# Performance work log

Hardware: AMD Instinct MI355X
Metric: run time of the kernel (lower is better)

## Reference

```python
import jax, jax.numpy as jnp
import numpy as np


def setup_inputs() -> dict:
    key = jax.random.key(0)
    k1, k2, k3, k4 = jax.random.split(key, 4)
    B, Lq, Lk, d = 8, 2048, 2048, 64
    queries = jax.random.normal(k1, (B, Lq, d), dtype=jnp.float32)
    keys = jax.random.normal(k2, (B, Lk, d), dtype=jnp.float32)
    values = jax.random.normal(k3, (B, Lk, d), dtype=jnp.float32)
    valid_lens = jax.random.randint(k4, (B,), 0, 2048, dtype=jnp.int64)
    return {"queries": queries, "keys": keys, "values": values, "valid_lens": valid_lens}


def reference(queries, keys, values, valid_lens):
    # scores: [B, Lq, Lk]
    d = queries.shape[-1]
    scale = 1.0 / jnp.sqrt(jnp.asarray(d, dtype=queries.dtype))
    scores = jnp.einsum("bqd,bkd->bqk", queries, keys) * scale
    # length mask: key positions >= valid_len[b] get -1e6 (as in sequence_mask)
    Lk = keys.shape[1]
    mask = jnp.arange(Lk)[None, None, :] < valid_lens[:, None, None]  # [B,1,Lk]
    scores = jnp.where(mask, scores, jnp.asarray(-1e6, dtype=scores.dtype))
    attn = jax.nn.softmax(scores, axis=-1)
    # dropout p=0.0 -> identity
    return jnp.einsum("bqk,bkd->bqd", attn, values)
```

## Files before the change

### kernel.cpp

```cpp
#include <hip/hip_runtime.h>
#include <hip/hip_bf16.h>
#include <math.h>

typedef __attribute__((ext_vector_type(8))) short short8;
typedef __attribute__((ext_vector_type(16))) float f32x16;

#define DHEAD 64
#define KVB 32
#define QB 32
#define NW 8
#define NWF 4

__device__ __forceinline__ unsigned pack2_bf16(float a, float b) {
  unsigned ua = __builtin_bit_cast(unsigned, a);
  unsigned ub = __builtin_bit_cast(unsigned, b);
  ua = (ua + 0x7fffu + ((ua >> 16) & 1u)) >> 16;
  ub = (ub + 0x7fffu + ((ub >> 16) & 1u)) >> 16;
  return (ua & 0xffffu) | (ub << 16);
}

union Frag { unsigned u[4]; short8 s; };

__global__ __launch_bounds__(256)
void prep_kv(const float* __restrict__ K, const float* __restrict__ V,
             unsigned short* __restrict__ Kf, unsigned short* __restrict__ Vf,
             const int* __restrict__ VL, int Lk) {
  __shared__ float Vs[32][65];
  const int b = blockIdx.y, t = blockIdx.x, tid = threadIdx.x;
  const int LkT = Lk / 32;
  const int vl = VL[b];
  int nkb = (vl == 0) ? LkT : ((vl + 31) / 32);
  if (nkb > LkT) nkb = LkT;
  if (t >= nkb) return;

  const int kk = tid >> 6, lane = tid & 63;
  const int row = lane & 31, colb = kk * 16 + ((lane >> 5) & 1) * 8;
  const size_t base = ((size_t)b * Lk + t * 32) * DHEAD;

  {
    const float* src = K + base + (size_t)row * DHEAD + colb;
    Frag fr;
    #pragma unroll
    for (int j = 0; j < 4; ++j)
      fr.u[j] = pack2_bf16(src[2 * j], src[2 * j + 1]);
    *(short8*)(Kf + ((size_t)(b * LkT + t)) * 2048 + tid * 8) = fr.s;
  }
  for (int e = tid; e < 32 * DHEAD; e += 256) Vs[e >> 6][e & 63] = V[base + e];
  __syncthreads();
  const int region = tid >> 6;
  const int vkk = region & 1, half = region >> 1;
  const int krow = vkk * 16 + ((lane >> 5) & 1) * 8;
  const int d = half * 32 + (lane & 31);
  Frag fv;
  #pragma unroll
  for (int j = 0; j < 4; ++j)
    fv.u[j] = pack2_bf16(Vs[krow + 2 * j][d], Vs[krow + 2 * j + 1][d]);
  *(short8*)(Vf + ((size_t)(b * LkT + t)) * 2048 + tid * 8) = fv.s;
}

__device__ __forceinline__ void tile_body(
    int t, int nkb, int vl, int lane, int hi,
    const unsigned short* __restrict__ kb, const unsigned short* __restrict__ vb,
    const short8 (&qf)[4], short8 (&kc)[4], short8 (&kn)[4],
    short8 (&vc)[4], short8 (&vn)[4],
    f32x16& o0, f32x16& o1, float& m, float& l) {
  const float MASKV = -1442695.04f;

  f32x16 s = {};
  __builtin_amdgcn_s_setprio(1);
  #pragma unroll
  for (int kk = 0; kk < 4; ++kk)
    s = __builtin_amdgcn_mfma_f32_32x32x16_bf16(kc[kk], qf[kk], s, 0, 0, 0);
  __builtin_amdgcn_s_setprio(0);

  const int tn = t + NW;
  if (tn < nkb) {
    const unsigned short* ktn = kb + (size_t)tn * 2048;
    const unsigned short* vtn = vb + (size_t)tn * 2048;
    #pragma unroll
    for (int kk = 0; kk < 4; ++kk) {
      kn[kk] = *(const short8*)(ktn + kk * 512 + lane * 8);
      vn[kk] = *(const short8*)(vtn + kk * 512 + lane * 8);
    }
  }

  const int key0 = t * KVB;
  if (key0 + KVB > vl) {
    #pragma unroll
    for (int r = 0; r < 16; ++r) {
      const int key = key0 + (r & 3) + 8 * (r >> 2) + 4 * hi;
      if (key >= vl) s[r] = MASKV;
    }
  }

  float t0 = fmaxf(s[0], s[1]),  t1 = fmaxf(s[2], s[3]);
  float t2 = fmaxf(s[4], s[5]),  t3 = fmaxf(s[6], s[7]);
  float t4 = fmaxf(s[8], s[9]),  t5 = fmaxf(s[10], s[11]);
  float t6 = fmaxf(s[12], s[13]), t7 = fmaxf(s[14], s[15]);
  t0 = fmaxf(t0, t1); t2 = fmaxf(t2, t3); t4 = fmaxf(t4, t5); t6 = fmaxf(t6, t7);
  t0 = fmaxf(t0, t2); t4 = fmaxf(t4, t6);
  float tm = fmaxf(t0, t4);
  tm = fmaxf(tm, __shfl_xor(tm, 32));

  if (__any(tm > m)) {
    const float mnew  = fmaxf(m, tm);
    const float alpha = exp2f(m - mnew);
    #pragma unroll
    for (int r = 0; r < 16; ++r) { o0[r] *= alpha; o1[r] *= alpha; }
    l *= alpha;
    m = mnew;
  }
  #pragma unroll
  for (int r = 0; r < 16; ++r) s[r] = exp2f(s[r] - m);
  float u0 = s[0] + s[1],  u1 = s[2] + s[3];
  float u2 = s[4] + s[5],  u3 = s[6] + s[7];
  float u4 = s[8] + s[9],  u5 = s[10] + s[11];
  float u6 = s[12] + s[13], u7 = s[14] + s[15];
  u0 += u1; u2 += u3; u4 += u5; u6 += u7; u0 += u2; u4 += u6;
  l += u0 + u4 + __shfl_xor(u0 + u4, 32);

  short8 pf[2];
  #pragma unroll
  for (int kk = 0; kk < 2; ++kk) {
    const unsigned A0 = pack2_bf16(s[8 * kk + 0], s[8 * kk + 1]);
    const unsigned B0 = pack2_bf16(s[8 * kk + 2], s[8 * kk + 3]);
    const unsigned C0 = pack2_bf16(s[8 * kk + 4], s[8 * kk + 5]);
    const unsigned D0 = pack2_bf16(s[8 * kk + 6], s[8 * kk + 7]);
    const unsigned sA = (unsigned)__shfl_xor((int)A0, 32);
    const unsigned sB = (unsigned)__shfl_xor((int)B0, 32);
    const unsigned sC = (unsigned)__shfl_xor((int)C0, 32);
    const unsigned sD = (unsigned)__shfl_xor((int)D0, 32);
    Frag fr;
    fr.u[0] = hi ? sC : A0;
    fr.u[1] = hi ? sD : B0;
    fr.u[2] = hi ? C0 : sA;
    fr.u[3] = hi ? D0 : sB;
    pf[kk] = fr.s;
  }

  __builtin_amdgcn_s_setprio(1);
  o0 = __builtin_amdgcn_mfma_f32_32x32x16_bf16(vc[0], pf[0], o0, 0, 0, 0);
  o1 = __builtin_amdgcn_mfma_f32_32x32x16_bf16(vc[2], pf[0], o1, 0, 0, 0);
  o0 = __builtin_amdgcn_mfma_f32_32x32x16_bf16(vc[1], pf[1], o0, 0, 0, 0);
  o1 = __builtin_amdgcn_mfma_f32_32x32x16_bf16(vc[3], pf[1], o1, 0, 0, 0);
  __builtin_amdgcn_s_setprio(0);
}

__global__ __launch_bounds__(NW * 64, 2)
void fa8(const float* __restrict__ Qg, const unsigned short* __restrict__ Kf,
         const unsigned short* __restrict__ Vf, const int* __restrict__ VL,
         float* __restrict__ Og, int Lq, int Lk, int nqt) {
  __shared__ float OLs[4][QB][DHEAD + 1];
  __shared__ float mL[4][QB];
  __shared__ float lL[4][QB];
  __shared__ float FIN[QB][DHEAD + 2];

  const int tid  = threadIdx.x;
  const int w    = tid >> 6;
  const int lane = tid & 63;
  const int l31  = lane & 31;
  const int hi   = lane >> 5;
  const int qt   = blockIdx.x;
  const int b    = blockIdx.y;
  const int vl   = VL[b];

  const int LkT = Lk / KVB;
  int nkb = (vl == 0) ? LkT : ((vl + KVB - 1) / KVB);
  if (nkb > LkT) nkb = LkT;

  const float cQ = 0.125f * 1.4426950408889634f;
  short8 qf[4];
  {
    const float* qrow = Qg + ((size_t)b * Lq + qt * QB + l31) * DHEAD + hi * 8;
    #pragma unroll
    for (int kk = 0; kk < 4; ++kk) {
      Frag fr;
      #pragma unroll
      for (int j = 0; j < 4; ++j)
        fr.u[j] = pack2_bf16(qrow[kk * 16 + 2 * j] * cQ,
                             qrow[kk * 16 + 2 * j + 1] * cQ);
      qf[kk] = fr.s;
    }
  }

  const unsigned short* kb = Kf + (size_t)b * LkT * 2048;
  const unsigned short* vb = Vf + (size_t)b * LkT * 2048;

  f32x16 o0 = {};
  f32x16 o1 = {};
  float m = -INFINITY;
  float l = 0.0f;

  int t = w;
  if (t < nkb) {
    short8 kA[4], kB[4], vA[4], vB[4];
    const unsigned short* kt = kb + (size_t)t * 2048;
    const unsigned short* vt = vb + (size_t)t * 2048;
    #pragma unroll
    for (int kk = 0; kk < 4; ++kk) {
      kA[kk] = *(const short8*)(kt + kk * 512 + lane * 8);
      vA[kk] = *(const short8*)(vt + kk * 512 + lane * 8);
    }
    while (true) {
      tile_body(t, nkb, vl, lane, hi, kb, vb, qf, kA, kB, vA, vB, o0, o1, m, l);
      t += NW; if (t >= nkb) break;
      tile_body(t, nkb, vl, lane, hi, kb, vb, qf, kB, kA, vB, vA, o0, o1, m, l);
      t += NW; if (t >= nkb) break;
    }
  }

  #pragma unroll
  for (int ph = 0; ph < 3; ++ph) {
    const int wlo  = (ph == 0) ? 4 : (ph == 1) ? 2 : 1;
    const int wcnt = wlo == 1 ? 1 : wlo;

    if (w >= wlo && w < wlo + wcnt) {
      const int s = w - wlo;
      if (hi == 0) { mL[s][l31] = m; lL[s][l31] = l; }
      #pragma unroll
      for (int r = 0; r < 16; ++r) {
        const int dr = (r & 3) + 8 * (r >> 2) + 4 * hi;
        OLs[s][l31][dr]      = o0[r];
        OLs[s][l31][dr + 32] = o1[r];
      }
    }
    __syncthreads();
    if (w < wcnt) {
      const int s = w;
      const float m2 = mL[s][l31];
      const float l2 = lL[s][l31];
      const float M  = fmaxf(m, m2);
      const float a  = (l  > 0.f) ? exp2f(m - M)  : 0.f;
      const float a2 = (l2 > 0.f) ? exp2f(m2 - M) : 0.f;
      #pragma unroll
      for (int r = 0; r < 16; ++r) {
        const int dr = (r & 3) + 8 * (r >> 2) + 4 * hi;
        o0[r] = o0[r] * a + OLs[s][l31][dr]      * a2;
        o1[r] = o1[r] * a + OLs[s][l31][dr + 32] * a2;
      }
      l = l * a + l2 * a2;
      m = M;
    }
    __syncthreads();
  }

  if (w == 0) {
    const float rl = (l > 0.f) ? 1.0f / l : 0.0f;
    #pragma unroll
    for (int r = 0; r < 16; ++r) {
      const int dr = (r & 3) + 8 * (r >> 2) + 4 * hi;
      FIN[l31][dr]      = o0[r] * rl;
      FIN[l31][dr + 32] = o1[r] * rl;
    }
  }
  __syncthreads();
  const size_t base = ((size_t)b * Lq + (size_t)qt * QB) * DHEAD;
  for (int e = tid; e < QB * DHEAD; e += NW * 64)
    Og[base + e] = FIN[e >> 6][e & 63];
}

__global__ __launch_bounds__(NWF * 64)
void fa_fwd(const float* __restrict__ Qg, const float* __restrict__ Kg,
            const float* __restrict__ Vg, const int* __restrict__ VL,
            float* __restrict__ Og, int Lq, int Lk) {
  __shared__ float OLs[NWF][QB][DHEAD + 1];
  __shared__ float mLs[NWF][QB];
  __shared__ float lLs[NWF][QB];

  const int tid  = threadIdx.x;
  const int w    = tid >> 6;
  const int lane = tid & 63;
  const int l31  = lane & 31;
  const int hi   = lane >> 5;
  const int q0   = blockIdx.x * QB;
  const int b    = blockIdx.y;
  const int vl   = VL[b];

  const float* Qb = Qg + (size_t)b * Lq * DHEAD;
  const float* Kb = Kg + (size_t)b * Lk * DHEAD;
  const float* Vb = Vg + (size_t)b * Lk * DHEAD;

  const float cQ = 0.125f * 1.4426950408889634f;
  short8 qf[4];
  {
    const float* qrow = Qb + (size_t)(q0 + l31) * DHEAD + hi * 8;
    #pragma unroll
    for (int kk = 0; kk < 4; ++kk) {
      Frag fr;
      #pragma unroll
      for (int j = 0; j < 4; ++j)
        fr.u[j] = pack2_bf16(qrow[kk * 16 + 2 * j] * cQ,
                             qrow[kk * 16 + 2 * j + 1] * cQ);
      qf[kk] = fr.s;
    }
  }

  f32x16 o0 = {};
  f32x16 o1 = {};
  float m = -INFINITY;
  float l = 0.0f;

  int nkb = (vl == 0) ? (Lk / KVB) : ((vl + KVB - 1) / KVB);
  if (nkb > Lk / KVB) nkb = Lk / KVB;
  const int nt = (nkb > w) ? ((nkb - w + NWF - 1) / NWF) : 0;

  const float MASKV = -1442695.04f;

  float kraw[32], vraw[32];

  if (nt > 0) {
    const float* krow = Kb + (size_t)(w * KVB + l31) * DHEAD + hi * 8;
    #pragma unroll
    for (int kk = 0; kk < 4; ++kk)
      #pragma unroll
      for (int j = 0; j < 8; ++j) kraw[kk * 8 + j] = krow[kk * 16 + j];
  }

  for (int t = 0; t < nt; ++t) {
    const int key0 = (w + t * NWF) * KVB;

    short8 kf[4];
    #pragma unroll
    for (int kk = 0; kk < 4; ++kk) {
      Frag fr;
      #pragma unroll
      for (int j = 0; j < 4; ++j)
        fr.u[j] = pack2_bf16(kraw[kk * 8 + 2 * j], kraw[kk * 8 + 2 * j + 1]);
      kf[kk] = fr.s;
    }

    #pragma unroll
    for (int kk = 0; kk < 2; ++kk) {
      const float* vrow = Vb + (size_t)(key0 + kk * 16 + hi * 8) * DHEAD + l31;
      #pragma unroll
      for (int j = 0; j < 8; ++j) {
        vraw[kk * 16 + j]     = vrow[j * DHEAD];
        vraw[kk * 16 + 8 + j] = vrow[j * DHEAD + 32];
      }
    }

    f32x16 s = {};
    #pragma unroll
    for (int kk = 0; kk < 4; ++kk)
      s = __builtin_amdgcn_mfma_f32_32x32x16_bf16(kf[kk], qf[kk], s, 0, 0, 0);

    if (t + 1 < nt) {
      const float* krow = Kb + (size_t)(key0 + NWF * KVB + l31) * DHEAD + hi * 8;
      #pragma unroll
      for (int kk = 0; kk < 4; ++kk)
        #pragma unroll
        for (int j = 0; j < 8; ++j) kraw[kk * 8 + j] = krow[kk * 16 + j];
    }

    if (key0 + KVB > vl) {
      #pragma unroll
      for (int r = 0; r < 16; ++r) {
        const int key = key0 + (r & 3) + 8 * (r >> 2) + 4 * hi;
        if (key >= vl) s[r] = MASKV;
      }
    }

    float t0 = fmaxf(s[0], s[1]),  t1 = fmaxf(s[2], s[3]);
    float t2 = fmaxf(s[4], s[5]),  t3 = fmaxf(s[6], s[7]);
    float t4 = fmaxf(s[8], s[9]),  t5 = fmaxf(s[10], s[11]);
    float t6 = fmaxf(s[12], s[13]), t7 = fmaxf(s[14], s[15]);
    t0 = fmaxf(t0, t1); t2 = fmaxf(t2, t3); t4 = fmaxf(t4, t5); t6 = fmaxf(t6, t7);
    t0 = fmaxf(t0, t2); t4 = fmaxf(t4, t6);
    float tm = fmaxf(t0, t4);
    tm = fmaxf(tm, __shfl_xor(tm, 32));
    const float mnew  = fmaxf(m, tm);
    const float alpha = exp2f(m - mnew);
    #pragma unroll
    for (int r = 0; r < 16; ++r) s[r] = exp2f(s[r] - mnew);
    float u0 = s[0] + s[1],  u1 = s[2] + s[3];
    float u2 = s[4] + s[5],  u3 = s[6] + s[7];
    float u4 = s[8] + s[9],  u5 = s[10] + s[11];
    float u6 = s[12] + s[13], u7 = s[14] + s[15];
    u0 += u1; u2 += u3; u4 += u5; u6 += u7; u0 += u2; u4 += u6;
    float sum = u0 + u4;
    sum += __shfl_xor(sum, 32);
    l = l * alpha + sum;
    m = mnew;
    #pragma unroll
    for (int r = 0; r < 16; ++r) { o0[r] *= alpha; o1[r] *= alpha; }

    short8 pf[2];
    #pragma unroll
    for (int kk = 0; kk < 2; ++kk) {
      const unsigned A0 = pack2_bf16(s[8 * kk + 0], s[8 * kk + 1]);
      const unsigned B0 = pack2_bf16(s[8 * kk + 2], s[8 * kk + 3]);
      const unsigned C0 = pack2_bf16(s[8 * kk + 4], s[8 * kk + 5]);
      const unsigned D0 = pack2_bf16(s[8 * kk + 6], s[8 * kk + 7]);
      const unsigned sA = (unsigned)__shfl_xor((int)A0, 32);
      const unsigned sB = (unsigned)__shfl_xor((int)B0, 32);
      const unsigned sC = (unsigned)__shfl_xor((int)C0, 32);
      const unsigned sD = (unsigned)__shfl_xor((int)D0, 32);
      Frag fr;
      fr.u[0] = hi ? sC : A0;
      fr.u[1] = hi ? sD : B0;
      fr.u[2] = hi ? C0 : sA;
      fr.u[3] = hi ? D0 : sB;
      pf[kk] = fr.s;
    }

    #pragma unroll
    for (int kk = 0; kk < 2; ++kk) {
      Frag f0, f1;
      #pragma unroll
      for (int j = 0; j < 4; ++j) {
        f0.u[j] = pack2_bf16(vraw[kk * 16 + 2 * j],     vraw[kk * 16 + 2 * j + 1]);
        f1.u[j] = pack2_bf16(vraw[kk * 16 + 8 + 2 * j], vraw[kk * 16 + 8 + 2 * j + 1]);
      }
      o0 = __builtin_amdgcn_mfma_f32_32x32x16_bf16(f0.s, pf[kk], o0, 0, 0, 0);
      o1 = __builtin_amdgcn_mfma_f32_32x32x16_bf16(f1.s, pf[kk], o1, 0, 0, 0);
    }
  }

  if (hi == 0) { mLs[w][l31] = m; lLs[w][l31] = l; }
  #pragma unroll
  for (int r = 0; r < 16; ++r) {
    const int dr = (r & 3) + 8 * (r >> 2) + 4 * hi;
    OLs[w][l31][dr]      = o0[r];
    OLs[w][l31][dr + 32] = o1[r];
  }
  __syncthreads();

  for (int e = tid; e < QB * DHEAD; e += NWF * 64) {
    const int q = e >> 6;
    const int d = e & 63;
    float M = mLs[0][q];
    #pragma unroll
    for (int ww = 1; ww < NWF; ++ww) M = fmaxf(M, mLs[ww][q]);
    float L = 0.f, acc = 0.f;
    #pragma unroll
    for (int ww = 0; ww < NWF; ++ww) {
      const float wgt = exp2f(mLs[ww][q] - M);
      L   += lLs[ww][q] * wgt;
      acc += OLs[ww][q][d] * wgt;
    }
    Og[((size_t)b * Lq + q0 + q) * DHEAD + d] = acc / L;
  }
}

extern "C" void kernel_launch(void* const* d_in, const int* in_sizes, int n_in,
                              void* d_out, int out_size, void* d_ws, size_t ws_size,
                              hipStream_t stream) {
  const float* Q  = (const float*)d_in[0];
  const float* K  = (const float*)d_in[1];
  const float* V  = (const float*)d_in[2];
  const int*   VL = (const int*)d_in[3];
  float* O = (float*)d_out;

  const int B  = in_sizes[3];
  const int Lq = in_sizes[0] / (B * DHEAD);
  const int Lk = in_sizes[1] / (B * DHEAD);
  const int nqt = Lq / QB;

  const size_t kfE = (size_t)B * Lk * DHEAD;
  const size_t need = kfE * 2 * 2;

  if (ws_size >= need) {
    unsigned short* Kf = (unsigned short*)d_ws;
    unsigned short* Vf = Kf + kfE;

    dim3 pgrid(Lk / 32, B);
    prep_kv<<<pgrid, 256, 0, stream>>>(K, V, Kf, Vf, VL, Lk);
    dim3 g1(nqt, B);
    fa8<<<g1, NW * 64, 0, stream>>>(Q, Kf, Vf, VL, O, Lq, Lk, nqt);
  } else {
    dim3 grid(Lq / QB, B);
    fa_fwd<<<grid, NWF * 64, 0, stream>>>(Q, K, V, VL, O, Lq, Lk);
  }
}
```

Baseline: 34.88 us.

## Process two query tiles per block to reuse each K/V tile

Each block now handles two 32-row query tiles and applies every loaded K and V fragment to both, halving K/V global traffic per query and halving the grid size. V is loaded at the start of each tile rather than prefetched one tile ahead, and the cross-wave reduction runs twice. This doubles accumulator register pressure and halves the number of blocks (from 512 to 256), which may reduce occupancy and latency hiding on a large GPU.

```diff
diff --git a/kernel.cpp b/kernel.cpp
--- a/kernel.cpp
+++ b/kernel.cpp
@@ -58,33 +58,10 @@
   *(short8*)(Vf + ((size_t)(b * LkT + t)) * 2048 + tid * 8) = fv.s;
 }
 
-__device__ __forceinline__ void tile_body(
-    int t, int nkb, int vl, int lane, int hi,
-    const unsigned short* __restrict__ kb, const unsigned short* __restrict__ vb,
-    const short8 (&qf)[4], short8 (&kc)[4], short8 (&kn)[4],
-    short8 (&vc)[4], short8 (&vn)[4],
+__device__ __forceinline__ void softmax_pv(
+    f32x16& s, const short8 (&vf)[4], int key0, int vl, int hi,
     f32x16& o0, f32x16& o1, float& m, float& l) {
   const float MASKV = -1442695.04f;
-
-  f32x16 s = {};
-  __builtin_amdgcn_s_setprio(1);
-  #pragma unroll
-  for (int kk = 0; kk < 4; ++kk)
-    s = __builtin_amdgcn_mfma_f32_32x32x16_bf16(kc[kk], qf[kk], s, 0, 0, 0);
-  __builtin_amdgcn_s_setprio(0);
-
-  const int tn = t + NW;
-  if (tn < nkb) {
-    const unsigned short* ktn = kb + (size_t)tn * 2048;
-    const unsigned short* vtn = vb + (size_t)tn * 2048;
-    #pragma unroll
-    for (int kk = 0; kk < 4; ++kk) {
-      kn[kk] = *(const short8*)(ktn + kk * 512 + lane * 8);
-      vn[kk] = *(const short8*)(vtn + kk * 512 + lane * 8);
-    }
-  }
-
-  const int key0 = t * KVB;
   if (key0 + KVB > vl) {
     #pragma unroll
     for (int r = 0; r < 16; ++r) {
@@ -92,7 +69,6 @@
       if (key >= vl) s[r] = MASKV;
     }
   }
-
   float t0 = fmaxf(s[0], s[1]),  t1 = fmaxf(s[2], s[3]);
   float t2 = fmaxf(s[4], s[5]),  t3 = fmaxf(s[6], s[7]);
   float t4 = fmaxf(s[8], s[9]),  t5 = fmaxf(s[10], s[11]);
@@ -139,17 +115,56 @@
   }
 
   __builtin_amdgcn_s_setprio(1);
-  o0 = __builtin_amdgcn_mfma_f32_32x32x16_bf16(vc[0], pf[0], o0, 0, 0, 0);
-  o1 = __builtin_amdgcn_mfma_f32_32x32x16_bf16(vc[2], pf[0], o1, 0, 0, 0);
-  o0 = __builtin_amdgcn_mfma_f32_32x32x16_bf16(vc[1], pf[1], o0, 0, 0, 0);
-  o1 = __builtin_amdgcn_mfma_f32_32x32x16_bf16(vc[3], pf[1], o1, 0, 0, 0);
+  o0 = __builtin_amdgcn_mfma_f32_32x32x16_bf16(vf[0], pf[0], o0, 0, 0, 0);
+  o1 = __builtin_amdgcn_mfma_f32_32x32x16_bf16(vf[2], pf[0], o1, 0, 0, 0);
+  o0 = __builtin_amdgcn_mfma_f32_32x32x16_bf16(vf[1], pf[1], o0, 0, 0, 0);
+  o1 = __builtin_amdgcn_mfma_f32_32x32x16_bf16(vf[3], pf[1], o1, 0, 0, 0);
   __builtin_amdgcn_s_setprio(0);
 }
 
+__device__ __forceinline__ void tile_body2(
+    int t, int nkb, int vl, int lane, int hi,
+    const unsigned short* __restrict__ kb, const unsigned short* __restrict__ vb,
+    const short8 (&qf0)[4], const short8 (&qf1)[4],
+    short8 (&kc)[4], short8 (&kn)[4],
+    f32x16& o0a, f32x16& o1a, float& m0, float& l0,
+    f32x16& o0b, f32x16& o1b, float& m1, float& l1) {
+  const unsigned short* vt = vb + (size_t)t * 2048;
+  short8 vf[4];
+  #pragma unroll
+  for (int kk = 0; kk < 4; ++kk)
+    vf[kk] = *(const short8*)(vt + kk * 512 + lane * 8);
+
+  f32x16 s0 = {}, s1 = {};
+  __builtin_amdgcn_s_setprio(1);
+  #pragma unroll
+  for (int kk = 0; kk < 4; ++kk)
+    s0 = __builtin_amdgcn_mfma_f32_32x32x16_bf16(kc[kk], qf0[kk], s0, 0, 0, 0);
+  __builtin_amdgcn_s_setprio(0);
+
+  const int tn = t + NW;
+  if (tn < nkb) {
+    const unsigned short* ktn = kb + (size_t)tn * 2048;
+    #pragma unroll
+    for (int kk = 0; kk < 4; ++kk)
+      kn[kk] = *(const short8*)(ktn + kk * 512 + lane * 8);
+  }
+
+  __builtin_amdgcn_s_setprio(1);
+  #pragma unroll
+  for (int kk = 0; kk < 4; ++kk)
+    s1 = __builtin_amdgcn_mfma_f32_32x32x16_bf16(kc[kk], qf1[kk], s1, 0, 0, 0);
+  __builtin_amdgcn_s_setprio(0);
+
+  const int key0 = t * KVB;
+  softmax_pv(s0, vf, key0, vl, hi, o0a, o1a, m0, l0);
+  softmax_pv(s1, vf, key0, vl, hi, o0b, o1b, m1, l1);
+}
+
 __global__ __launch_bounds__(NW * 64, 2)
-void fa8(const float* __restrict__ Qg, const unsigned short* __restrict__ Kf,
-         const unsigned short* __restrict__ Vf, const int* __restrict__ VL,
-         float* __restrict__ Og, int Lq, int Lk, int nqt) {
+void fa2q(const float* __restrict__ Qg, const unsigned short* __restrict__ Kf,
+          const unsigned short* __restrict__ Vf, const int* __restrict__ VL,
+          float* __restrict__ Og, int Lq, int Lk, int nqt) {
   __shared__ float OLs[4][QB][DHEAD + 1];
   __shared__ float mL[4][QB];
   __shared__ float lL[4][QB];
@@ -160,7 +175,9 @@
   const int lane = tid & 63;
   const int l31  = lane & 31;
   const int hi   = lane >> 5;
-  const int qt   = blockIdx.x;
+  const int qt0  = blockIdx.x * 2;
+  const int qt1  = qt0 + 1;
+  const bool hasQ1 = (qt1 < nqt);
   const int b    = blockIdx.y;
   const int vl   = VL[b];
 
@@ -169,94 +186,108 @@
   if (nkb > LkT) nkb = LkT;
 
   const float cQ = 0.125f * 1.4426950408889634f;
-  short8 qf[4];
+  short8 qf0[4], qf1[4];
   {
-    const float* qrow = Qg + ((size_t)b * Lq + qt * QB + l31) * DHEAD + hi * 8;
+    const float* q0row = Qg + ((size_t)b * Lq + qt0 * QB + l31) * DHEAD + hi * 8;
+    const float* q1row = Qg + ((size_t)b * Lq + (hasQ1 ? qt1 : qt0) * QB + l31) * DHEAD + hi * 8;
     #pragma unroll
     for (int kk = 0; kk < 4; ++kk) {
-      Frag fr;
-      #pragma unroll
-      for (int j = 0; j < 4; ++j)
-        fr.u[j] = pack2_bf16(qrow[kk * 16 + 2 * j] * cQ,
-                             qrow[kk * 16 + 2 * j + 1] * cQ);
-      qf[kk] = fr.s;
+      Frag f0, f1;
+      #pragma unroll
+      for (int j = 0; j < 4; ++j) {
+        f0.u[j] = pack2_bf16(q0row[kk * 16 + 2 * j] * cQ, q0row[kk * 16 + 2 * j + 1] * cQ);
+        f1.u[j] = pack2_bf16(q1row[kk * 16 + 2 * j] * cQ, q1row[kk * 16 + 2 * j + 1] * cQ);
+      }
+      qf0[kk] = f0.s;
+      qf1[kk] = f1.s;
     }
   }
 
   const unsigned short* kb = Kf + (size_t)b * LkT * 2048;
   const unsigned short* vb = Vf + (size_t)b * LkT * 2048;
 
-  f32x16 o0 = {};
-  f32x16 o1 = {};
-  float m = -INFINITY;
-  float l = 0.0f;
+  f32x16 o0a = {}, o1a = {};
+  f32x16 o0b = {}, o1b = {};
+  float m0 = -INFINITY, l0 = 0.0f;
+  float m1 = -INFINITY, l1 = 0.0f;
 
   int t = w;
   if (t < nkb) {
-    short8 kA[4], kB[4], vA[4], vB[4];
+    short8 kA[4], kB[4];
     const unsigned short* kt = kb + (size_t)t * 2048;
-    const unsigned short* vt = vb + (size_t)t * 2048;
-    #pragma unroll
-    for (int kk = 0; kk < 4; ++kk) {
+    #pragma unroll
+    for (int kk = 0; kk < 4; ++kk)
       kA[kk] = *(const short8*)(kt + kk * 512 + lane * 8);
-      vA[kk] = *(const short8*)(vt + kk * 512 + lane * 8);
-    }
     while (true) {
-      tile_body(t, nkb, vl, lane, hi, kb, vb, qf, kA, kB, vA, vB, o0, o1, m, l);
+      tile_body2(t, nkb, vl, lane, hi, kb, vb, qf0, qf1, kA, kB,
+                 o0a, o1a, m0, l0, o0b, o1b, m1, l1);
       t += NW; if (t >= nkb) break;
-      tile_body(t, nkb, vl, lane, hi, kb, vb, qf, kB, kA, vB, vA, o0, o1, m, l);
+      tile_body2(t, nkb, vl, lane, hi, kb, vb, qf0, qf1, kB, kA,
+                 o0a, o1a, m0, l0, o0b, o1b, m1, l1);
       t += NW; if (t >= nkb) break;
     }
   }
 
   #pragma unroll
-  for (int ph = 0; ph < 3; ++ph) {
-    const int wlo  = (ph == 0) ? 4 : (ph == 1) ? 2 : 1;
-    const int wcnt = wlo == 1 ? 1 : wlo;
-
-    if (w >= wlo && w < wlo + wcnt) {
-      const int s = w - wlo;
-      if (hi == 0) { mL[s][l31] = m; lL[s][l31] = l; }
+  for (int qp = 0; qp < 2; ++qp) {
+    f32x16& o0 = (qp == 0) ? o0a : o0b;
+    f32x16& o1 = (qp == 0) ? o1a : o1b;
+    float&  m  = (qp == 0) ? m0  : m1;
+    float&  l  = (qp == 0) ? l0  : l1;
+    const int qt = (qp == 0) ? qt0 : qt1;
+
+    #pragma unroll
+    for (int ph = 0; ph < 3; ++ph) {
+      const int wlo  = (ph == 0) ? 4 : (ph == 1) ? 2 : 1;
+      const int wcnt = wlo == 1 ? 1 : wlo;
+
+      if (w >= wlo && w < wlo + wcnt) {
+        const int s = w - wlo;
+        if (hi == 0) { mL[s][l31] = m; lL[s][l31] = l; }
+        #pragma unroll
+        for (int r = 0; r < 16; ++r) {
+          const int dr = (r & 3) + 8 * (r >> 2) + 4 * hi;
+          OLs[s][l31][dr]      = o0[r];
+          OLs[s][l31][dr + 32] = o1[r];
+        }
+      }
+      __syncthreads();
+      if (w < wcnt) {
+        const int s = w;
+        const float m2 = mL[s][l31];
+        const float l2 = lL[s][l31];
+        const float M  = fmaxf(m, m2);
+        const float a  = (l  > 0.f) ? exp2f(m - M)  : 0.f;
+        const float a2 = (l2 > 0.f) ? exp2f(m2 - M) : 0.f;
+        #pragma unroll
+        for (int r = 0; r < 16; ++r) {
+          const int dr = (r & 3) + 8 * (r >> 2) + 4 * hi;
+          o0[r] = o0[r] * a + OLs[s][l31][dr]      * a2;
+          o1[r] = o1[r] * a + OLs[s][l31][dr + 32] * a2;
+        }
+        l = l * a + l2 * a2;
+        m = M;
+      }
+      __syncthreads();
+    }
+
+    if (w == 0) {
+      const float rl = (l > 0.f) ? 1.0f / l : 0.0f;
       #pragma unroll
       for (int r = 0; r < 16; ++r) {
         const int dr = (r & 3) + 8 * (r >> 2) + 4 * hi;
-        OLs[s][l31][dr]      = o0[r];
-        OLs[s][l31][dr + 32] = o1[r];
+        FIN[l31][dr]      = o0[r] * rl;
+        FIN[l31][dr + 32] = o1[r] * rl;
       }
     }
     __syncthreads();
-    if (w < wcnt) {
-      const int s = w;
-      const float m2 = mL[s][l31];
-      const float l2 = lL[s][l31];
-      const float M  = fmaxf(m, m2);
-      const float a  = (l  > 0.f) ? exp2f(m - M)  : 0.f;
-      const float a2 = (l2 > 0.f) ? exp2f(m2 - M) : 0.f;
-      #pragma unroll
-      for (int r = 0; r < 16; ++r) {
-        const int dr = (r & 3) + 8 * (r >> 2) + 4 * hi;
-        o0[r] = o0[r] * a + OLs[s][l31][dr]      * a2;
-        o1[r] = o1[r] * a + OLs[s][l31][dr + 32] * a2;
-      }
-      l = l * a + l2 * a2;
-      m = M;
+    if (qp == 0 || hasQ1) {
+      const size_t base = ((size_t)b * Lq + (size_t)qt * QB) * DHEAD;
+      for (int e = tid; e < QB * DHEAD; e += NW * 64)
+        Og[base + e] = FIN[e >> 6][e & 63];
     }
     __syncthreads();
   }
-
-  if (w == 0) {
-    const float rl = (l > 0.f) ? 1.0f / l : 0.0f;
-    #pragma unroll
-    for (int r = 0; r < 16; ++r) {
-      const int dr = (r & 3) + 8 * (r >> 2) + 4 * hi;
-      FIN[l31][dr]      = o0[r] * rl;
-      FIN[l31][dr + 32] = o1[r] * rl;
-    }
-  }
-  __syncthreads();
-  const size_t base = ((size_t)b * Lq + (size_t)qt * QB) * DHEAD;
-  for (int e = tid; e < QB * DHEAD; e += NW * 64)
-    Og[base + e] = FIN[e >> 6][e & 63];
 }
 
 __global__ __launch_bounds__(NWF * 64)
@@ -465,8 +496,8 @@
 
     dim3 pgrid(Lk / 32, B);
     prep_kv<<<pgrid, 256, 0, stream>>>(K, V, Kf, Vf, VL, Lk);
-    dim3 g1(nqt, B);
-    fa8<<<g1, NW * 64, 0, stream>>>(Q, Kf, Vf, VL, O, Lq, Lk, nqt);
+    dim3 g1((nqt + 1) / 2, B);
+    fa2q<<<g1, NW * 64, 0, stream>>>(Q, Kf, Vf, VL, O, Lq, Lk, nqt);
   } else {
     dim3 grid(Lq / QB, B);
     fa_fwd<<<grid, NWF * 64, 0, stream>>>(Q, K, V, VL, O, Lq, Lk);
```

Result: slower. 38.56 us (+10.5%).
